# Kernel tuning notes

Measured on AMD Instinct MI355X. Metric: run time of the kernel, lower is better.

Reference implementation:

```python
import jax, jax.numpy as jnp
import numpy as np

EMBED_DIM = 384
N_DOCS = 262144
BATCH = 64
TOP_K = 8
EPS = 1e-8


def setup_inputs() -> dict:
    key = jax.random.key(0)
    kq, kd = jax.random.split(key)
    query = jax.random.normal(kq, (BATCH, EMBED_DIM), dtype=jnp.float32)
    doc_embeddings = jax.random.normal(kd, (N_DOCS, EMBED_DIM), dtype=jnp.float32)
    return {"query": query, "doc_embeddings": doc_embeddings, "top_k": TOP_K}


def reference(query, doc_embeddings, top_k):
    # Cosine similarity: L2-normalize both sides.
    qn = query / (jnp.linalg.norm(query, axis=-1, keepdims=True) + EPS)          # [B, d]
    dn = doc_embeddings / (jnp.linalg.norm(doc_embeddings, axis=-1, keepdims=True) + EPS)  # [N, d]
    # Similarity scores between every query and every document.
    scores = jnp.einsum('bd,nd->bn', qn, dn)                                      # [B, N]
    # Top-k retrieval.
    topk_scores, topk_idx = jax.lax.top_k(scores, top_k)                          # [B, k]
    # Gather retrieved document embeddings.
    retrieved = dn[topk_idx]                                                      # [B, k, d]
    # Context fusion: softmax-weighted sum of retrieved docs.
    weights = jax.nn.softmax(topk_scores, axis=-1)                                # [B, k]
    fused = jnp.einsum('bk,bkd->bd', weights, retrieved)                          # [B, d]
    return fused, topk_scores, topk_idx
```

## Files before the change

### kernel.cpp

```cpp
#include <hip/hip_runtime.h>
#include <math.h>


#define EMBED 384
#define NDOCS 262144
#define BATCH 64
#define TOPK 8
#define DBLK 256
#define NBLK (NDOCS / DBLK)
#define EPSN 1e-8f
#define SCW 260

typedef __attribute__((ext_vector_type(8))) short bf16x8;
typedef __attribute__((ext_vector_type(4))) float f32x4;

#define INS8(s_, i_) do {                                                     \
    if ((s_) > ts[7] || ((s_) == ts[7] && (i_) < ti[7])) {                    \
        ts[7] = (s_); ti[7] = (i_);                                           \
        _Pragma("unroll")                                                     \
        for (int r_ = 7; r_ > 0; --r_) {                                      \
            bool sw_ = (ts[r_] > ts[r_-1]) ||                                 \
                       (ts[r_] == ts[r_-1] && ti[r_] < ti[r_-1]);             \
            float a_ = ts[r_-1]; int b_ = ti[r_-1];                           \
            ts[r_-1] = sw_ ? ts[r_] : a_;  ti[r_-1] = sw_ ? ti[r_] : b_;      \
            ts[r_]   = sw_ ? a_ : ts[r_];  ti[r_]   = sw_ ? b_ : ti[r_];      \
        }                                                                     \
    }                                                                         \
} while (0)

template<int OFF>
__device__ __forceinline__ int4 gload16o(const void* p) {
    int4 r;
    asm volatile("global_load_dwordx4 %0, %1, off offset:%2"
                 : "=v"(r) : "v"(p), "i"(OFF) : "memory");
    return r;
}

__device__ __forceinline__ void split8v(f32x4 f0, f32x4 f1, bf16x8& bh, bf16x8& bl) {
    float f[8] = {f0[0], f0[1], f0[2], f0[3], f1[0], f1[1], f1[2], f1[3]};
#pragma unroll
    for (int i = 0; i < 8; ++i) {
        unsigned u = __float_as_uint(f[i]);
        unsigned h = (u + 0x7fffu + ((u >> 16) & 1u)) >> 16;
        float fh = __uint_as_float(h << 16);
        float r = f[i] - fh;
        unsigned v = __float_as_uint(r);
        unsigned lo = (v + 0x7fffu + ((v >> 16) & 1u)) >> 16;
        bh[i] = (short)h;
        bl[i] = (short)lo;
    }
}

__device__ __forceinline__ float dot8v(f32x4 f0, f32x4 f1, float s) {
#pragma unroll
    for (int i = 0; i < 4; ++i) s = fmaf(f0[i], f0[i], s);
#pragma unroll
    for (int i = 0; i < 4; ++i) s = fmaf(f1[i], f1[i], s);
    return s;
}

__global__ void qprep_kernel(const float* __restrict__ q,
                             unsigned short* __restrict__ qh,
                             unsigned short* __restrict__ ql) {
    const int row = blockIdx.x;
    const int lane = threadIdx.x;
    float v[6];
    float s = 0.f;
#pragma unroll
    for (int i = 0; i < 6; ++i) {
        v[i] = q[row * EMBED + lane + 64 * i];
        s = fmaf(v[i], v[i], s);
    }
#pragma unroll
    for (int off = 32; off > 0; off >>= 1) s += __shfl_xor(s, off);
    float rinv = 1.0f / (sqrtf(s) + EPSN);
#pragma unroll
    for (int i = 0; i < 6; ++i) {
        float f = v[i] * rinv;
        unsigned u = __float_as_uint(f);
        unsigned h = (u + 0x7fffu + ((u >> 16) & 1u)) >> 16;
        float fh = __uint_as_float(h << 16);
        float r = f - fh;
        unsigned vv = __float_as_uint(r);
        unsigned lo = (vv + 0x7fffu + ((vv >> 16) & 1u)) >> 16;
        qh[row * EMBED + lane + 64 * i] = (unsigned short)h;
        ql[row * EMBED + lane + 64 * i] = (unsigned short)lo;
    }
}

__global__ __launch_bounds__(256, 2) void score_topk_kernel(
        const float* __restrict__ docs,
        const unsigned short* __restrict__ qh,
        const unsigned short* __restrict__ ql,
        float* __restrict__ pscore, int* __restrict__ pidx) {
    __shared__ float S[BATCH * SCW];

    const int tid = threadIdx.x;
    const int l = tid & 63;
    const int wv = tid >> 6;
    const int rowl = l & 15;
    const int ksub = l >> 4;
    const int d0 = blockIdx.x * DBLK;

    f32x4 acc[4][4];
#pragma unroll
    for (int s = 0; s < 4; ++s)
#pragma unroll
        for (int m = 0; m < 4; ++m) acc[s][m] = (f32x4){0.f, 0.f, 0.f, 0.f};
    float sq[4] = {0.f, 0.f, 0.f, 0.f};

    const float* dbase[4];
#pragma unroll
    for (int s = 0; s < 4; ++s)
        dbase[s] = docs + (size_t)(d0 + wv * 64 + s * 16 + rowl) * EMBED + ksub * 8;
    const unsigned short* qb_[8];
#pragma unroll
    for (int m = 0; m < 4; ++m) {
        qb_[m]     = qh + (m * 16 + rowl) * EMBED + ksub * 8;
        qb_[4 + m] = ql + (m * 16 + rowl) * EMBED + ksub * 8;
    }

    int4 qA[8], qB[8], dA[8], dB[8];

#pragma unroll
    for (int m = 0; m < 8; ++m) qA[m] = gload16o<0>(qb_[m]);
#pragma unroll
    for (int s = 0; s < 4; ++s) {
        dA[2 * s]     = gload16o<0>(dbase[s]);
        dA[2 * s + 1] = gload16o<16>(dbase[s]);
    }

#define ITER(KB, QC, DC, QN, DN, PF, VM)                                       \
    {                                                                          \
        if (PF) {                                                              \
            _Pragma("unroll")                                                  \
            for (int m = 0; m < 8; ++m)                                        \
                QN[m] = gload16o<((KB) + 1) * 64>(qb_[m]);                     \
            _Pragma("unroll")                                                  \
            for (int s = 0; s < 4; ++s) {                                      \
                DN[2 * s]     = gload16o<((KB) + 1) * 128>(dbase[s]);          \
                DN[2 * s + 1] = gload16o<((KB) + 1) * 128 + 16>(dbase[s]);     \
            }                                                                  \
        }                                                                      \
        asm volatile("s_waitcnt " VM ::: "memory");                            \
        __builtin_amdgcn_sched_barrier(0);                                     \
        _Pragma("unroll")                                                      \
        for (int s = 0; s < 4; ++s) {                                          \
            f32x4 fa = *(f32x4*)&DC[2 * s];                                    \
            f32x4 fb = *(f32x4*)&DC[2 * s + 1];                                \
            sq[s] = dot8v(fa, fb, sq[s]);                                      \
            bf16x8 bh, bl;                                                     \
            split8v(fa, fb, bh, bl);                                           \
            _Pragma("unroll")                                                  \
            for (int m = 0; m < 4; ++m) {                                      \
                bf16x8 ah = *(bf16x8*)&QC[m];                                  \
                bf16x8 al = *(bf16x8*)&QC[4 + m];                              \
                acc[s][m] = __builtin_amdgcn_mfma_f32_16x16x32_bf16(ah, bh, acc[s][m], 0, 0, 0); \
                acc[s][m] = __builtin_amdgcn_mfma_f32_16x16x32_bf16(al, bh, acc[s][m], 0, 0, 0); \
                acc[s][m] = __builtin_amdgcn_mfma_f32_16x16x32_bf16(ah, bl, acc[s][m], 0, 0, 0); \
            }                                                                  \
        }                                                                      \
    }

    ITER(0,  qA, dA, qB, dB, 1, "vmcnt(16)")
    ITER(1,  qB, dB, qA, dA, 1, "vmcnt(16)")
    ITER(2,  qA, dA, qB, dB, 1, "vmcnt(16)")
    ITER(3,  qB, dB, qA, dA, 1, "vmcnt(16)")
    ITER(4,  qA, dA, qB, dB, 1, "vmcnt(16)")
    ITER(5,  qB, dB, qA, dA, 1, "vmcnt(16)")
    ITER(6,  qA, dA, qB, dB, 1, "vmcnt(16)")
    ITER(7,  qB, dB, qA, dA, 1, "vmcnt(16)")
    ITER(8,  qA, dA, qB, dB, 1, "vmcnt(16)")
    ITER(9,  qB, dB, qA, dA, 1, "vmcnt(16)")
    ITER(10, qA, dA, qB, dB, 1, "vmcnt(16)")
    ITER(11, qB, dB, qA, dA, 0, "vmcnt(0)")
#undef ITER

#pragma unroll
    for (int s = 0; s < 4; ++s) {
        float t = sq[s];
        t += __shfl_xor(t, 16);
        t += __shfl_xor(t, 32);
        float rn = 1.0f / (sqrtf(t) + EPSN);
        const int col = wv * 64 + s * 16 + rowl;
        const int q0 = ksub * 4;
#pragma unroll
        for (int m = 0; m < 4; ++m) {
            f32x4 a = acc[s][m];
#pragma unroll
            for (int j = 0; j < 4; ++j)
                S[(m * 16 + q0 + j) * SCW + col] = a[j] * rn;
        }
    }
    __syncthreads();

    float ts[8]; int ti[8];
#pragma unroll
    for (int r = 0; r < 8; ++r) { ts[r] = -3.402823466e38f; ti[r] = 0x7fffffff; }
    const int q = tid & 63, qa = tid >> 6;
    for (int ii = 0; ii < 64; ++ii) {
        int d = qa * 64 + ((ii + q) & 63);
        float sc = S[q * SCW + d];
        INS8(sc, d0 + d);
    }
    __syncthreads();
#pragma unroll
    for (int r = 0; r < 8; ++r) {
        S[(qa * 64 + q) * 8 + r] = ts[r];
        S[2048 + (qa * 64 + q) * 8 + r] = __int_as_float(ti[r]);
    }
    __syncthreads();
    if (tid < 64) {
#pragma unroll
        for (int r = 0; r < 8; ++r) { ts[r] = -3.402823466e38f; ti[r] = 0x7fffffff; }
        for (int a = 0; a < 4; ++a) {
#pragma unroll
            for (int r = 0; r < 8; ++r) {
                float s2 = S[(a * 64 + q) * 8 + r];
                int i2 = __float_as_int(S[2048 + (a * 64 + q) * 8 + r]);
                INS8(s2, i2);
            }
        }
        size_t o = ((size_t)q * NBLK + blockIdx.x) * TOPK;
        *(float4*)&pscore[o]     = make_float4(ts[0], ts[1], ts[2], ts[3]);
        *(float4*)&pscore[o + 4] = make_float4(ts[4], ts[5], ts[6], ts[7]);
        *(int4*)&pidx[o]     = make_int4(ti[0], ti[1], ti[2], ti[3]);
        *(int4*)&pidx[o + 4] = make_int4(ti[4], ti[5], ti[6], ti[7]);
    }
}

__global__ __launch_bounds__(256) void merge_a_kernel(
        const float* __restrict__ pscore, const int* __restrict__ pidx,
        float* __restrict__ cs, int* __restrict__ ci) {
    const int q = blockIdx.x >> 2;
    const int c = blockIdx.x & 3;
    const int tid = threadIdx.x;
    __shared__ float ls[2048];
    __shared__ int   li[2048];
    __shared__ float ls2[512];
    __shared__ int   li2[512];
    __shared__ float ls3[64];
    __shared__ int   li3[64];

    {
        size_t o = ((size_t)q * NBLK + c * 256 + tid) * TOPK;
        float4 s0 = *(const float4*)&pscore[o];
        float4 s1 = *(const float4*)&pscore[o + 4];
        int4 i0 = *(const int4*)&pidx[o];
        int4 i1 = *(const int4*)&pidx[o + 4];
        ls[tid * 8 + 0] = s0.x; ls[tid * 8 + 1] = s0.y;
        ls[tid * 8 + 2] = s0.z; ls[tid * 8 + 3] = s0.w;
        ls[tid * 8 + 4] = s1.x; ls[tid * 8 + 5] = s1.y;
        ls[tid * 8 + 6] = s1.z; ls[tid * 8 + 7] = s1.w;
        li[tid * 8 + 0] = i0.x; li[tid * 8 + 1] = i0.y;
        li[tid * 8 + 2] = i0.z; li[tid * 8 + 3] = i0.w;
        li[tid * 8 + 4] = i1.x; li[tid * 8 + 5] = i1.y;
        li[tid * 8 + 6] = i1.z; li[tid * 8 + 7] = i1.w;
    }
    __syncthreads();

    float ts[8]; int ti[8];
    if (tid < 64) {
#pragma unroll
        for (int r = 0; r < 8; ++r) { ts[r] = -3.402823466e38f; ti[r] = 0x7fffffff; }
        for (int e = 0; e < 32; ++e) {
            int k = tid + e * 64;
            float s = ls[k]; int gi = li[k];
            INS8(s, gi);
        }
#pragma unroll
        for (int r = 0; r < 8; ++r) { ls2[tid * 8 + r] = ts[r]; li2[tid * 8 + r] = ti[r]; }
    }
    __syncthreads();
    if (tid < 8) {
#pragma unroll
        for (int r = 0; r < 8; ++r) { ts[r] = -3.402823466e38f; ti[r] = 0x7fffffff; }
        for (int e = 0; e < 64; ++e) {
            int k = tid + e * 8;
            float s = ls2[k]; int gi = li2[k];
            INS8(s, gi);
        }
#pragma unroll
        for (int r = 0; r < 8; ++r) { ls3[tid * 8 + r] = ts[r]; li3[tid * 8 + r] = ti[r]; }
    }
    __syncthreads();
    if (tid == 0) {
#pragma unroll
        for (int r = 0; r < 8; ++r) { ts[r] = -3.402823466e38f; ti[r] = 0x7fffffff; }
        for (int e = 0; e < 64; ++e) {
            float s = ls3[e]; int gi = li3[e];
            INS8(s, gi);
        }
        size_t o = (size_t)(q * 4 + c) * TOPK;
#pragma unroll
        for (int r = 0; r < 8; ++r) { cs[o + r] = ts[r]; ci[o + r] = ti[r]; }
    }
}

__global__ __launch_bounds__(256) void merge_b_kernel(
        const float* __restrict__ docs, const float* __restrict__ cs,
        const int* __restrict__ ci, float* __restrict__ out) {
    const int q = blockIdx.x;
    const int tid = threadIdx.x;
    __shared__ int   fi[TOPK];
    __shared__ float wr[TOPK];

    if (tid == 0) {
        float ts[8]; int ti[8];
#pragma unroll
        for (int r = 0; r < 8; ++r) { ts[r] = -3.402823466e38f; ti[r] = 0x7fffffff; }
        for (int e = 0; e < 32; ++e) {
            float s = cs[q * 32 + e]; int gi = ci[q * 32 + e];
            INS8(s, gi);
        }
        float m = ts[0];
        float w[8]; float sum = 0.f;
#pragma unroll
        for (int r = 0; r < 8; ++r) { w[r] = expf(ts[r] - m); sum += w[r]; }
        float rs = 1.0f / sum;
#pragma unroll
        for (int r = 0; r < 8; ++r) {
            fi[r] = ti[r];
            wr[r] = w[r] * rs;
            out[BATCH * EMBED + q * TOPK + r] = ts[r];
            out[BATCH * EMBED + BATCH * TOPK + q * TOPK + r] = (float)ti[r];
        }
    }
    __syncthreads();

    int lane = tid & 63, wave = tid >> 6;
    for (int r = wave; r < TOPK; r += 4) {
        const float* dp = docs + (size_t)fi[r] * EMBED;
        float s = 0.f;
#pragma unroll
        for (int i = 0; i < 6; ++i) { float v = dp[lane + 64 * i]; s = fmaf(v, v, s); }
#pragma unroll
        for (int off = 32; off > 0; off >>= 1) s += __shfl_xor(s, off);
        if (lane == 0) wr[r] = wr[r] / (sqrtf(s) + EPSN);
    }
    __syncthreads();

    for (int dim = tid; dim < EMBED; dim += 256) {
        float a = 0.f;
#pragma unroll
        for (int r = 0; r < 8; ++r)
            a += wr[r] * docs[(size_t)fi[r] * EMBED + dim];
        out[q * EMBED + dim] = a;
    }
}

extern "C" void kernel_launch(void* const* d_in, const int* in_sizes, int n_in,
                              void* d_out, int out_size, void* d_ws, size_t ws_size,
                              hipStream_t stream) {
    const float* query = (const float*)d_in[0];
    const float* docs  = (const float*)d_in[1];
    float* out = (float*)d_out;

    char* ws = (char*)d_ws;
    unsigned short* qh = (unsigned short*)ws;
    unsigned short* ql = (unsigned short*)(ws + 49152);
    float* pscore = (float*)(ws + 98304);
    int*   pidx   = (int*)(ws + 98304 + (size_t)NBLK * BATCH * TOPK * 4);
    char*  ws3    = ws + 98304 + 2 * (size_t)NBLK * BATCH * TOPK * 4;
    float* cs     = (float*)ws3;
    int*   ci     = (int*)(ws3 + BATCH * 4 * TOPK * 4);

    qprep_kernel<<<64, 64, 0, stream>>>(query, qh, ql);
    score_topk_kernel<<<NBLK, 256, 0, stream>>>(docs, qh, ql, pscore, pidx);
    merge_a_kernel<<<BATCH * 4, 256, 0, stream>>>(pscore, pidx, cs, ci);
    merge_b_kernel<<<BATCH, 256, 0, stream>>>(docs, cs, ci, out);
}
```

Before: 238.9 us.

## Split doc tiles once into LDS and share across waves; hold queries in registers

Before, each wave loaded its own 64 documents plus all 64 query rows per k-step and did the bf16 hi/lo split on its own doc slice. Now each wave owns 16 query rows for the whole K range, preloaded into registers. Doc tiles are loaded coalesced and split once per block, then written to LDS as hi/lo bf16 tiles that all waves read with ds_read_b128. This removes repeated global query loads and gives every wave reuse of all 256 docs, at the cost of two __syncthreads per k-step, 66 KB of shared memory, larger register pressure, and a vmcnt(0) wait per step that limits overlap.

```diff
diff --git a/kernel.cpp b/kernel.cpp
--- a/kernel.cpp
+++ b/kernel.cpp
@@ -10,6 +10,8 @@
 #define NBLK (NDOCS / DBLK)
 #define EPSN 1e-8f
 #define SCW 260
+#define LO_OFF 20480u
+#define RN_OFF 66560
 
 typedef __attribute__((ext_vector_type(8))) short bf16x8;
 typedef __attribute__((ext_vector_type(4))) float f32x4;
@@ -29,34 +31,38 @@
 } while (0)
 
 template<int OFF>
-__device__ __forceinline__ int4 gload16o(const void* p) {
+__device__ __forceinline__ int4 gload_s(unsigned voff, const void* sbase) {
     int4 r;
-    asm volatile("global_load_dwordx4 %0, %1, off offset:%2"
-                 : "=v"(r) : "v"(p), "i"(OFF) : "memory");
+    asm volatile("global_load_dwordx4 %0, %1, %2 offset:%3"
+                 : "=v"(r) : "v"(voff), "s"(sbase), "i"(OFF) : "memory");
     return r;
 }
 
-__device__ __forceinline__ void split8v(f32x4 f0, f32x4 f1, bf16x8& bh, bf16x8& bl) {
-    float f[8] = {f0[0], f0[1], f0[2], f0[3], f1[0], f1[1], f1[2], f1[3]};
-#pragma unroll
-    for (int i = 0; i < 8; ++i) {
-        unsigned u = __float_as_uint(f[i]);
-        unsigned h = (u + 0x7fffu + ((u >> 16) & 1u)) >> 16;
-        float fh = __uint_as_float(h << 16);
-        float r = f[i] - fh;
-        unsigned v = __float_as_uint(r);
-        unsigned lo = (v + 0x7fffu + ((v >> 16) & 1u)) >> 16;
-        bh[i] = (short)h;
-        bl[i] = (short)lo;
-    }
-}
-
-__device__ __forceinline__ float dot8v(f32x4 f0, f32x4 f1, float s) {
-#pragma unroll
-    for (int i = 0; i < 4; ++i) s = fmaf(f0[i], f0[i], s);
-#pragma unroll
-    for (int i = 0; i < 4; ++i) s = fmaf(f1[i], f1[i], s);
-    return s;
+__device__ __forceinline__ int4 dsread16(unsigned a) {
+    int4 r;
+    asm volatile("ds_read_b128 %0, %1" : "=v"(r) : "v"(a) : "memory");
+    return r;
+}
+
+#define SPB(F, H, O) {                                                        \
+    unsigned u_ = __float_as_uint(F);                                         \
+    H = (u_ + 0x7fffu + ((u_ >> 16) & 1u)) >> 16;                             \
+    float r_ = (F) - __uint_as_float((H) << 16);                              \
+    unsigned v_ = __float_as_uint(r_);                                        \
+    O = (v_ + 0x7fffu + ((v_ >> 16) & 1u)) >> 16;                             \
+}
+
+#define SPLIT4(J) {                                                           \
+    f32x4 f_ = *(f32x4*)&ld[J];                                               \
+    nacc[J] = fmaf(f_[0], f_[0], fmaf(f_[1], f_[1],                           \
+              fmaf(f_[2], f_[2], fmaf(f_[3], f_[3], nacc[J]))));              \
+    unsigned h0_, h1_, h2_, h3_, o0_, o1_, o2_, o3_;                          \
+    SPB(f_[0], h0_, o0_); SPB(f_[1], h1_, o1_);                               \
+    SPB(f_[2], h2_, o2_); SPB(f_[3], h3_, o3_);                               \
+    sh[J].x = (h0_ & 0xffffu) | (h1_ << 16);                                  \
+    sh[J].y = (h2_ & 0xffffu) | (h3_ << 16);                                  \
+    sl[J].x = (o0_ & 0xffffu) | (o1_ << 16);                                  \
+    sl[J].y = (o2_ & 0xffffu) | (o3_ << 16);                                  \
 }
 
 __global__ void qprep_kernel(const float* __restrict__ q,
@@ -77,12 +83,8 @@
 #pragma unroll
     for (int i = 0; i < 6; ++i) {
         float f = v[i] * rinv;
-        unsigned u = __float_as_uint(f);
-        unsigned h = (u + 0x7fffu + ((u >> 16) & 1u)) >> 16;
-        float fh = __uint_as_float(h << 16);
-        float r = f - fh;
-        unsigned vv = __float_as_uint(r);
-        unsigned lo = (vv + 0x7fffu + ((vv >> 16) & 1u)) >> 16;
+        unsigned h, lo;
+        SPB(f, h, lo);
         qh[row * EMBED + lane + 64 * i] = (unsigned short)h;
         ql[row * EMBED + lane + 64 * i] = (unsigned short)lo;
     }
@@ -93,104 +95,120 @@
         const unsigned short* __restrict__ qh,
         const unsigned short* __restrict__ ql,
         float* __restrict__ pscore, int* __restrict__ pidx) {
-    __shared__ float S[BATCH * SCW];
+    __shared__ __align__(16) char smem[67584];
+    float* S  = (float*)smem;
+    float* RN = (float*)(smem + RN_OFF);
 
     const int tid = threadIdx.x;
-    const int l = tid & 63;
-    const int wv = tid >> 6;
+    const int l   = tid & 63;
+    const int wv  = tid >> 6;
     const int rowl = l & 15;
     const int ksub = l >> 4;
     const int d0 = blockIdx.x * DBLK;
-
-    f32x4 acc[4][4];
-#pragma unroll
-    for (int s = 0; s < 4; ++s)
-#pragma unroll
-        for (int m = 0; m < 4; ++m) acc[s][m] = (f32x4){0.f, 0.f, 0.f, 0.f};
-    float sq[4] = {0.f, 0.f, 0.f, 0.f};
-
-    const float* dbase[4];
-#pragma unroll
-    for (int s = 0; s < 4; ++s)
-        dbase[s] = docs + (size_t)(d0 + wv * 64 + s * 16 + rowl) * EMBED + ksub * 8;
-    const unsigned short* qb_[8];
-#pragma unroll
-    for (int m = 0; m < 4; ++m) {
-        qb_[m]     = qh + (m * 16 + rowl) * EMBED + ksub * 8;
-        qb_[4 + m] = ql + (m * 16 + rowl) * EMBED + ksub * 8;
-    }
-
-    int4 qA[8], qB[8], dA[8], dB[8];
-
-#pragma unroll
-    for (int m = 0; m < 8; ++m) qA[m] = gload16o<0>(qb_[m]);
-#pragma unroll
-    for (int s = 0; s < 4; ++s) {
-        dA[2 * s]     = gload16o<0>(dbase[s]);
-        dA[2 * s + 1] = gload16o<16>(dbase[s]);
-    }
-
-#define ITER(KB, QC, DC, QN, DN, PF, VM)                                       \
+    const unsigned bse = (unsigned)(uintptr_t)smem;
+
+    f32x4 acc[16];
+#pragma unroll
+    for (int s = 0; s < 16; ++s) acc[s] = (f32x4){0.f, 0.f, 0.f, 0.f};
+    float nacc[8];
+#pragma unroll
+    for (int j = 0; j < 8; ++j) nacc[j] = 0.f;
+
+    int4 qf[12][2];
+    {
+        unsigned vq = (unsigned)((wv * 16 + rowl) * (EMBED * 2) + ksub * 16);
+#pragma unroll
+        for (int kb = 0; kb < 12; ++kb) {
+            qf[kb][0] = gload_s<0>(vq, qh);
+            qf[kb][1] = gload_s<0>(vq, ql);
+            vq += 64;
+        }
+    }
+
+    unsigned voff[8];
+#pragma unroll
+    for (int j = 0; j < 8; ++j)
+        voff[j] = (unsigned)((d0 + wv * 64 + j * 8 + (l >> 3)) * 1536u)
+                + (unsigned)((l & 7) * 16);
+
+    int4 ld[8];
+#pragma unroll
+    for (int j = 0; j < 8; ++j) ld[j] = gload_s<0>(voff[j], docs);
+
+    uint2 sh[8], sl[8];
+    asm volatile("s_waitcnt vmcnt(0)" ::: "memory");
+    __builtin_amdgcn_sched_barrier(0);
+#pragma unroll
+    for (int j = 0; j < 8; ++j) SPLIT4(j);
+
+    const unsigned wbase = wv * 5120u + (unsigned)((l >> 3) * 80 + (l & 7) * 8);
+    const unsigned rbase = (unsigned)(rowl * 80 + ksub * 16);
+
+#define KITER(KB, LAST) {                                                      \
+    __syncthreads();                                \
+    _Pragma("unroll")                                                          \
+    for (int j = 0; j < 8; ++j) {                                              \
+        *(uint2*)(smem + wbase + j * 640u) = sh[j];                            \
+        *(uint2*)(smem + LO_OFF + wbase + j * 640u) = sl[j];                   \
+    }                                                                          \
+    __syncthreads();                                        \
+    if (!(LAST)) {                                                             \
+        _Pragma("unroll")                                                      \
+        for (int j = 0; j < 8; ++j)                                            \
+            ld[j] = gload_s<((KB) + 1) * 128>(voff[j], docs);                  \
+    }                                                                          \
     {                                                                          \
-        if (PF) {                                                              \
-            _Pragma("unroll")                                                  \
-            for (int m = 0; m < 8; ++m)                                        \
-                QN[m] = gload16o<((KB) + 1) * 64>(qb_[m]);                     \
-            _Pragma("unroll")                                                  \
-            for (int s = 0; s < 4; ++s) {                                      \
-                DN[2 * s]     = gload16o<((KB) + 1) * 128>(dbase[s]);          \
-                DN[2 * s + 1] = gload16o<((KB) + 1) * 128 + 16>(dbase[s]);     \
+        int4 fh0, fl0, fh1, fl1;                                               \
+        fh0 = dsread16(bse + rbase);                                           \
+        fl0 = dsread16(bse + rbase + LO_OFF);                                  \
+        _Pragma("unroll")                                                      \
+        for (int s = 0; s < 16; ++s) {                                         \
+            if (s < 15) {                                                      \
+                fh1 = dsread16(bse + rbase + (unsigned)((s + 1) * 1280));      \
+                fl1 = dsread16(bse + rbase + (unsigned)((s + 1) * 1280) + LO_OFF); \
+                asm volatile("s_waitcnt lgkmcnt(2)" ::: "memory");             \
+            } else {                                                           \
+                asm volatile("s_waitcnt lgkmcnt(0)" ::: "memory");             \
             }                                                                  \
+            __builtin_amdgcn_sched_barrier(0);                                 \
+            bf16x8 bh = *(bf16x8*)&fh0, bl = *(bf16x8*)&fl0;                   \
+            bf16x8 ah = *(bf16x8*)&qf[KB][0], al = *(bf16x8*)&qf[KB][1];       \
+            acc[s] = __builtin_amdgcn_mfma_f32_16x16x32_bf16(ah, bh, acc[s], 0, 0, 0); \
+            acc[s] = __builtin_amdgcn_mfma_f32_16x16x32_bf16(al, bh, acc[s], 0, 0, 0); \
+            acc[s] = __builtin_amdgcn_mfma_f32_16x16x32_bf16(ah, bl, acc[s], 0, 0, 0); \
+            fh0 = fh1; fl0 = fl1;                                              \
         }                                                                      \
-        asm volatile("s_waitcnt " VM ::: "memory");                            \
+    }                                                                          \
+    if (!(LAST)) {                                                             \
+        asm volatile("s_waitcnt vmcnt(0)" ::: "memory");                       \
         __builtin_amdgcn_sched_barrier(0);                                     \
         _Pragma("unroll")                                                      \
-        for (int s = 0; s < 4; ++s) {                                          \
-            f32x4 fa = *(f32x4*)&DC[2 * s];                                    \
-            f32x4 fb = *(f32x4*)&DC[2 * s + 1];                                \
-            sq[s] = dot8v(fa, fb, sq[s]);                                      \
-            bf16x8 bh, bl;                                                     \
-            split8v(fa, fb, bh, bl);                                           \
-            _Pragma("unroll")                                                  \
-            for (int m = 0; m < 4; ++m) {                                      \
-                bf16x8 ah = *(bf16x8*)&QC[m];                                  \
-                bf16x8 al = *(bf16x8*)&QC[4 + m];                              \
-                acc[s][m] = __builtin_amdgcn_mfma_f32_16x16x32_bf16(ah, bh, acc[s][m], 0, 0, 0); \
-                acc[s][m] = __builtin_amdgcn_mfma_f32_16x16x32_bf16(al, bh, acc[s][m], 0, 0, 0); \
-                acc[s][m] = __builtin_amdgcn_mfma_f32_16x16x32_bf16(ah, bl, acc[s][m], 0, 0, 0); \
-            }                                                                  \
-        }                                                                      \
-    }
-
-    ITER(0,  qA, dA, qB, dB, 1, "vmcnt(16)")
-    ITER(1,  qB, dB, qA, dA, 1, "vmcnt(16)")
-    ITER(2,  qA, dA, qB, dB, 1, "vmcnt(16)")
-    ITER(3,  qB, dB, qA, dA, 1, "vmcnt(16)")
-    ITER(4,  qA, dA, qB, dB, 1, "vmcnt(16)")
-    ITER(5,  qB, dB, qA, dA, 1, "vmcnt(16)")
-    ITER(6,  qA, dA, qB, dB, 1, "vmcnt(16)")
-    ITER(7,  qB, dB, qA, dA, 1, "vmcnt(16)")
-    ITER(8,  qA, dA, qB, dB, 1, "vmcnt(16)")
-    ITER(9,  qB, dB, qA, dA, 1, "vmcnt(16)")
-    ITER(10, qA, dA, qB, dB, 1, "vmcnt(16)")
-    ITER(11, qB, dB, qA, dA, 0, "vmcnt(0)")
-#undef ITER
-
-#pragma unroll
-    for (int s = 0; s < 4; ++s) {
-        float t = sq[s];
-        t += __shfl_xor(t, 16);
-        t += __shfl_xor(t, 32);
-        float rn = 1.0f / (sqrtf(t) + EPSN);
-        const int col = wv * 64 + s * 16 + rowl;
-        const int q0 = ksub * 4;
-#pragma unroll
-        for (int m = 0; m < 4; ++m) {
-            f32x4 a = acc[s][m];
-#pragma unroll
-            for (int j = 0; j < 4; ++j)
-                S[(m * 16 + q0 + j) * SCW + col] = a[j] * rn;
-        }
+        for (int j = 0; j < 8; ++j) SPLIT4(j);                                 \
+    }                                                                          \
+}
+
+    KITER(0, 0)  KITER(1, 0)  KITER(2, 0)  KITER(3, 0)
+    KITER(4, 0)  KITER(5, 0)  KITER(6, 0)  KITER(7, 0)
+    KITER(8, 0)  KITER(9, 0)  KITER(10, 0) KITER(11, 1)
+#undef KITER
+
+#pragma unroll
+    for (int j = 0; j < 8; ++j) {
+        float t = nacc[j];
+        t += __shfl_xor(t, 1);
+        t += __shfl_xor(t, 2);
+        t += __shfl_xor(t, 4);
+        if ((l & 7) == 0)
+            RN[wv * 64 + j * 8 + (l >> 3)] = 1.0f / (sqrtf(t) + EPSN);
+    }
+    __syncthreads();
+
+#pragma unroll
+    for (int s = 0; s < 16; ++s) {
+        float rn = RN[s * 16 + rowl];
+#pragma unroll
+        for (int jj = 0; jj < 4; ++jj)
+            S[(wv * 16 + ksub * 4 + jj) * SCW + s * 16 + rowl] = acc[s][jj] * rn;
     }
     __syncthreads();
 
```

Result: no change. 237.6 us (-0.6%).
